# Performance work log

Hardware: AMD Instinct MI355X
Metric: run time of the kernel (lower is better)

Reference implementation:

```python
import jax, jax.numpy as jnp
import numpy as np

B, S, H, NH = 2, 2048, 1024, 16
HD = H // NH  # 64


def setup_inputs() -> dict:
    key = jax.random.key(0)
    ks = jax.random.split(key, 12)
    sc = 0.02
    return {
        "query": jax.random.normal(ks[0], (B, S, H), dtype=jnp.float32),
        "key": jax.random.normal(ks[1], (B, S, H), dtype=jnp.float32),
        "value": jax.random.normal(ks[2], (B, S, H), dtype=jnp.float32),
        "attention_mask": jnp.zeros((B, S, S), dtype=jnp.float32),
        "Wq": jax.random.normal(ks[3], (H, H), dtype=jnp.float32) * sc,
        "bq": jnp.zeros((H,), dtype=jnp.float32),
        "Wk": jax.random.normal(ks[4], (H, H), dtype=jnp.float32) * sc,
        "bk": jnp.zeros((H,), dtype=jnp.float32),
        "Wv": jax.random.normal(ks[5], (H, H), dtype=jnp.float32) * sc,
        "bv": jnp.zeros((H,), dtype=jnp.float32),
        "Wo": jax.random.normal(ks[6], (H, H), dtype=jnp.float32) * sc,
        "bo": jnp.zeros((H,), dtype=jnp.float32),
    }


def reference(query, key, value, attention_mask, Wq, bq, Wk, bk, Wv, bv, Wo, bo):
    b = query.shape[0]
    # linear projections
    q = query @ Wq + bq
    k = key @ Wk + bk
    v = value @ Wv + bv
    # [b, s, h] -> [b, nh, s, hd]
    def split_heads(x):
        return x.reshape(b, -1, NH, HD).transpose(0, 2, 1, 3)
    q, k, v = split_heads(q), split_heads(k), split_heads(v)
    # scaled dot-product attention with materialized score matrix (faithful)
    scores = jnp.einsum("bhqd,bhkd->bhqk", q, k) / jnp.sqrt(jnp.float32(HD))
    scores = scores + attention_mask[:, None, :, :]
    weights = jax.nn.softmax(scores, axis=-1)  # dropout p=0 (eval)
    out = jnp.einsum("bhqk,bhkd->bhqd", weights, v)
    out = out.transpose(0, 2, 1, 3).reshape(b, -1, H)
    return out @ Wo + bo
```

## Files before the change

### kernel.cpp

```cpp
#include <hip/hip_runtime.h>
#include <hip/hip_bf16.h>
#include <math.h>

#define S_  2048
#define H_  1024
#define NH_ 16
#define HD_ 64
#define MM  4096
#define NB_ 2
#define NT_ (S_ / 64)
#define LOG2E 1.44269504088896340736f
#define SMFIX 32.0f

typedef __attribute__((ext_vector_type(8))) short bf16x8;
typedef __attribute__((ext_vector_type(4))) float f32x4;
typedef __attribute__((ext_vector_type(16))) float f32x16;
typedef __attribute__((ext_vector_type(4))) unsigned short us4;
typedef __attribute__((ext_vector_type(8))) unsigned short us8;
typedef __attribute__((ext_vector_type(2))) unsigned uint2v;

__device__ __forceinline__ void gld_lds16(const void* g, void* l) {
    __builtin_amdgcn_global_load_lds(
        (const __attribute__((address_space(1))) unsigned int*)g,
        (__attribute__((address_space(3))) unsigned int*)l, 16, 0, 0);
}

__device__ __forceinline__ unsigned short f2bf(float f) {
    union { float f; unsigned int u; } v; v.f = f;
    unsigned int r = v.u + 0x7FFFu + ((v.u >> 16) & 1u);
    return (unsigned short)(r >> 16);
}

__device__ __forceinline__ unsigned pkbf(float lo, float hi) {
    __hip_bfloat162 h = __float22bfloat162_rn(make_float2(lo, hi));
    unsigned u; __builtin_memcpy(&u, &h, 4); return u;
}

__device__ __forceinline__ float exp2_fast(float x) {
    float r; asm("v_exp_f32 %0, %1" : "=v"(r) : "v"(x)); return r;
}

__global__ __launch_bounds__(256)
void cvt_bf16_3(const float* __restrict__ s0, const float* __restrict__ s1,
                const float* __restrict__ s2, unsigned short* __restrict__ d0,
                unsigned short* __restrict__ d1, unsigned short* __restrict__ d2,
                int n8)
{
    const int z = blockIdx.y;
    const float* s = z == 0 ? s0 : z == 1 ? s1 : s2;
    unsigned short* d = z == 0 ? d0 : z == 1 ? d1 : d2;
    int i = blockIdx.x * 256 + threadIdx.x;
    if (i >= n8) return;
    float4 a = ((const float4*)s)[i * 2];
    float4 b = ((const float4*)s)[i * 2 + 1];
    union { unsigned u[4]; us8 v; } o;
    o.u[0] = pkbf(a.x, a.y); o.u[1] = pkbf(a.z, a.w);
    o.u[2] = pkbf(b.x, b.y); o.u[3] = pkbf(b.z, b.w);
    ((us8*)d)[i] = o.v;
}

__global__ __launch_bounds__(256)
void wtr_kernel(const float* __restrict__ W0, const float* __restrict__ W1,
                const float* __restrict__ W2, const float* __restrict__ W3,
                unsigned short* __restrict__ T0, unsigned short* __restrict__ T1,
                unsigned short* __restrict__ T2, unsigned short* __restrict__ T3)
{
    __shared__ float t[32][33];
    const float* W = blockIdx.z == 0 ? W0 : blockIdx.z == 1 ? W1 : blockIdx.z == 2 ? W2 : W3;
    unsigned short* T = blockIdx.z == 0 ? T0 : blockIdx.z == 1 ? T1 : blockIdx.z == 2 ? T2 : T3;
    const int n0 = blockIdx.x * 32, k0 = blockIdx.y * 32;
    const int tx = threadIdx.x & 31, ty = threadIdx.x >> 5;
    #pragma unroll
    for (int u = 0; u < 4; u++)
        t[ty + u * 8][tx] = W[(size_t)(k0 + ty + u * 8) * H_ + n0 + tx];
    __syncthreads();
    #pragma unroll
    for (int u = 0; u < 4; u++)
        T[(size_t)(n0 + ty + u * 8) * H_ + k0 + tx] = f2bf(t[tx][ty + u * 8]);
}

__global__ __launch_bounds__(256)
void mtr_kernel(const float* __restrict__ M, unsigned short* __restrict__ MT2)
{
    __shared__ float t[64][33];
    const int q0 = blockIdx.x * 64, t2 = blockIdx.y, b = blockIdx.z;
    const int kv0 = (t2 >> 1) * 64 + (t2 & 1) * 32;
    const float* Mb = M + (size_t)b * S_ * S_;
    const int tid = threadIdx.x;

    #pragma unroll
    for (int u = 0; u < 2; u++) {
        const int f4 = tid + u * 256;
        const int r = f4 >> 3, c = (f4 & 7) * 4;
        float4 v = *(const float4*)(Mb + (size_t)(q0 + r) * S_ + kv0 + c);
        t[r][c + 0] = v.x; t[r][c + 1] = v.y; t[r][c + 2] = v.z; t[r][c + 3] = v.w;
    }
    __syncthreads();

    const int lg2 = tid >> 7, rem = tid & 127;
    const int q = rem >> 1, half = rem & 1;
    union { unsigned u[4]; us8 v; } o;
    #pragma unroll
    for (int w = 0; w < 4; w++) {
        const int i0 = half * 8 + 2 * w;
        const int kc0 = (i0 & 3) + 8 * (i0 >> 2) + 4 * lg2;
        const int i1 = i0 + 1;
        const int kc1 = (i1 & 3) + 8 * (i1 >> 2) + 4 * lg2;
        o.u[w] = pkbf(fmaf(t[q][kc0], LOG2E, -SMFIX),
                      fmaf(t[q][kc1], LOG2E, -SMFIX));
    }
    const size_t flat = ((((size_t)b * 64 + t2) * 2 + lg2) * 2048 + (q0 + q)) * 16 + half * 8;
    *(us8*)(MT2 + flat) = o.v;
}

__device__ __forceinline__
void gemm_body(const unsigned short* __restrict__ A, const unsigned short* __restrict__ Bt,
               const float* __restrict__ bias, void* __restrict__ out, float scale, int epi)
{
    __shared__ __align__(16) unsigned short As[128 * 64];
    __shared__ __align__(16) unsigned short Bs[128 * 64];

    const int tid = threadIdx.x;
    const int lane = tid & 63, w = tid >> 6;
    const int lane16 = lane & 15, lg = lane >> 4;
    const int wm = w & 1, wn = w >> 1;
    const int n0 = blockIdx.x * 128, m0 = blockIdx.y * 128;

    f32x4 acc[4][4];
    #pragma unroll
    for (int m = 0; m < 4; m++)
        #pragma unroll
        for (int n = 0; n < 4; n++) acc[m][n] = (f32x4){0.f, 0.f, 0.f, 0.f};

    auto stage = [&](int kt) {
        #pragma unroll
        for (int u = 0; u < 4; u++) {
            const int seg = w * 4 + u;
            const int L = seg * 1024 + lane * 16;
            const int row = L >> 7;
            const int blk = (L >> 4) & 7;
            const int goff = kt * 64 + ((blk ^ (row & 7)) << 3);
            gld_lds16(A  + (size_t)(m0 + row) * 1024 + goff, (char*)As + L);
            gld_lds16(Bt + (size_t)(n0 + row) * 1024 + goff, (char*)Bs + L);
        }
    };

    stage(0);
    for (int kt = 0; kt < 16; kt++) {
        __syncthreads();
        #pragma unroll
        for (int ks = 0; ks < 2; ks++) {
            const int kb = ks * 64 + lg * 16;
            bf16x8 a[4], b[4];
            #pragma unroll
            for (int m = 0; m < 4; m++) {
                const int row = wm * 64 + m * 16 + lane16;
                a[m] = *(const bf16x8*)((const char*)As + row * 128 + (kb ^ ((row & 7) << 4)));
            }
            #pragma unroll
            for (int n = 0; n < 4; n++) {
                const int row = wn * 64 + n * 16 + lane16;
                b[n] = *(const bf16x8*)((const char*)Bs + row * 128 + (kb ^ ((row & 7) << 4)));
            }
            #pragma unroll
            for (int m = 0; m < 4; m++)
                #pragma unroll
                for (int n = 0; n < 4; n++)
                    acc[m][n] = __builtin_amdgcn_mfma_f32_16x16x32_bf16(a[m], b[n], acc[m][n], 0, 0, 0);
        }
        __syncthreads();
        if (kt + 1 < 16) stage(kt + 1);
    }

    #pragma unroll
    for (int n = 0; n < 4; n++) {
        const int col = n0 + wn * 64 + n * 16 + lane16;
        const float bs = bias[col];
        #pragma unroll
        for (int m = 0; m < 4; m++) {
            const int rowb = m0 + wm * 64 + m * 16 + lg * 4;
            if (epi == 0) {
                const int nh = col >> 6, hd = col & 63;
                #pragma unroll
                for (int j = 0; j < 4; j++) {
                    const int row = rowb + j;
                    const int bb = row >> 11, s = row & 2047;
                    ((unsigned short*)out)[((((size_t)bb * NH_ + nh) * S_ + s) << 6) + hd] =
                        f2bf((acc[m][n][j] + bs) * scale);
                }
            } else if (epi == 1) {
                const int nh = col >> 6, hd = col & 63;
                const int bb = rowb >> 11, s = rowb & 2047;
                us4 o;
                #pragma unroll
                for (int j = 0; j < 4; j++) o[j] = f2bf(acc[m][n][j] + bs);
                *(us4*)&((unsigned short*)out)[((((size_t)bb * NH_ + nh) * HD_ + hd) << 11) + s] = o;
            } else {
                #pragma unroll
                for (int j = 0; j < 4; j++)
                    ((float*)out)[(size_t)(rowb + j) * H_ + col] = acc[m][n][j] + bs;
            }
        }
    }
}

__global__ __launch_bounds__(256)
void gemm_qkv(const unsigned short* __restrict__ Xq, const unsigned short* __restrict__ Xk,
              const unsigned short* __restrict__ Xv,
              const unsigned short* __restrict__ Wtq, const unsigned short* __restrict__ Wtk,
              const unsigned short* __restrict__ Wtv,
              const float* __restrict__ bq, const float* __restrict__ bk,
              const float* __restrict__ bv,
              unsigned short* __restrict__ qh, unsigned short* __restrict__ kh,
              unsigned short* __restrict__ vt, float qscale)
{
    const int z = blockIdx.z;
    const unsigned short* A  = z == 0 ? Xq : z == 1 ? Xk : Xv;
    const unsigned short* Bt = z == 0 ? Wtq : z == 1 ? Wtk : Wtv;
    const float* bias        = z == 0 ? bq : z == 1 ? bk : bv;
    void* out                = z == 0 ? (void*)qh : z == 1 ? (void*)kh : (void*)vt;
    gemm_body(A, Bt, bias, out, z == 0 ? qscale : 1.0f, z == 2 ? 1 : 0);
}

__global__ __launch_bounds__(256)
void gemm_out(const unsigned short* __restrict__ A, const unsigned short* __restrict__ Bt,
              const float* __restrict__ bias, float* __restrict__ out)
{
    gemm_body(A, Bt, bias, out, 1.0f, 2);
}

__global__ __launch_bounds__(256, 2)
void mfma_attn(const unsigned short* __restrict__ qh, const unsigned short* __restrict__ kh,
               const unsigned short* __restrict__ vt, const unsigned short* __restrict__ maskT,
               unsigned short* __restrict__ ao)
{
    __shared__ __align__(16) unsigned short Ks[2][64 * 64];
    __shared__ __align__(16) unsigned short Vs[2][64 * 64];

    const int tid = threadIdx.x;
    const int lane = tid & 63, wq = tid >> 6;
    const int l31 = lane & 31, lg2 = lane >> 5;
    const int qt = blockIdx.x, h = blockIdx.y, bz = blockIdx.z;
    const int q = qt * 128 + wq * 32 + l31;

    const unsigned short* Kb = kh + ((size_t)(bz * NH_ + h) * S_) * HD_;
    const unsigned short* Vb = vt + ((size_t)(bz * NH_ + h) * HD_) * S_;
    const unsigned short* MT2b = maskT + (size_t)bz * S_ * S_;

    bf16x8 qfrag[4];
    {
        const unsigned short* Qrow = qh + (((size_t)(bz * NH_ + h) * S_) + q) * HD_;
        #pragma unroll
        for (int s = 0; s < 4; s++)
            qfrag[s] = *(const bf16x8*)(Qrow + s * 16 + lg2 * 8);
    }

    auto stageKV = [&](int t) {
        const int buf = t & 1;
        #pragma unroll
        for (int u = 0; u < 2; u++) {
            const int L = u * 4096 + tid * 16;
            const int row = L >> 7, blk = (L >> 4) & 7;
            const int off = (blk ^ (row & 7)) << 3;
            gld_lds16(Kb + (size_t)(t * 64 + row) * HD_ + off, (char*)&Ks[buf][0] + L);
            gld_lds16(Vb + (size_t)row * S_ + t * 64 + off,    (char*)&Vs[buf][0] + L);
        }
    };
    stageKV(0);

    us8 mpA[2][2], mpB[2][2];
    auto loadMT = [&](int t, us8 (&mp)[2][2]) {
        #pragma unroll
        for (int bb = 0; bb < 2; bb++) {
            const unsigned short* src = MT2b +
                ((((size_t)(t * 2 + bb)) * 2 + lg2) * 2048 + q) * 16;
            mp[bb][0] = *(const us8*)(src);
            mp[bb][1] = *(const us8*)(src + 8);
        }
    };
    loadMT(0, mpA);

    __syncthreads();

    f32x16 oacc[2];
    #pragma unroll
    for (int db = 0; db < 2; db++)
        #pragma unroll
        for (int i = 0; i < 16; i++) oacc[db][i] = 0.f;
    float l_run = 0.f;

    auto tile = [&](int t, us8 (&Mc)[2][2], us8 (&Mn)[2][2]) {
        if (t) __syncthreads();
        const int buf = t & 1;

        if (t + 1 < NT_) { stageKV(t + 1); loadMT(t + 1, Mn); }

        f32x16 sc[2];
        __builtin_amdgcn_s_setprio(1);
        #pragma unroll
        for (int bb = 0; bb < 2; bb++) {
            f32x16 a;
            #pragma unroll
            for (int i = 0; i < 16; i++) a[i] = 0.f;
            #pragma unroll
            for (int s = 0; s < 4; s++) {
                const int row = bb * 32 + l31;
                bf16x8 kf = *(const bf16x8*)((const char*)&Ks[buf][0] + row * 128 +
                                             ((s * 32 + lg2 * 16) ^ ((row & 7) << 4)));
                a = __builtin_amdgcn_mfma_f32_32x32x16_bf16(kf, qfrag[s], a, 0, 0, 0);
            }
            sc[bb] = a;
        }
        __builtin_amdgcn_s_setprio(0);

        #pragma unroll
        for (int bb = 0; bb < 2; bb++) {
            union { us8 v; unsigned u[4]; } h0, h1;
            h0.v = Mc[bb][0]; h1.v = Mc[bb][1];
            #pragma unroll
            for (int i = 0; i < 16; i++) {
                const unsigned wrd = (i < 8) ? h0.u[i >> 1] : h1.u[(i - 8) >> 1];
                const float mf = __uint_as_float((i & 1) ? (wrd & 0xFFFF0000u)
                                                         : (wrd << 16));
                sc[bb][i] = exp2_fast(sc[bb][i] + mf);
            }
        }
        float s8[8];
        #pragma unroll
        for (int i = 0; i < 8; i++)
            s8[i] = (sc[0][i] + sc[0][i + 8]) + (sc[1][i] + sc[1][i + 8]);
        l_run += ((s8[0] + s8[1]) + (s8[2] + s8[3])) + ((s8[4] + s8[5]) + (s8[6] + s8[7]));

        bf16x8 pfrag[4];
        #pragma unroll
        for (int bb = 0; bb < 2; bb++)
            #pragma unroll
            for (int g = 0; g < 2; g++) {
                const int o = g * 8;
                unsigned X0 = pkbf(sc[bb][o + 0], sc[bb][o + 1]);
                unsigned X1 = pkbf(sc[bb][o + 2], sc[bb][o + 3]);
                unsigned Y0 = pkbf(sc[bb][o + 4], sc[bb][o + 5]);
                unsigned Y1 = pkbf(sc[bb][o + 6], sc[bb][o + 7]);
                uint2v r0 = __builtin_amdgcn_permlane32_swap(X0, Y0, false, false);
                uint2v r1 = __builtin_amdgcn_permlane32_swap(X1, Y1, false, false);
                union { unsigned u[4]; bf16x8 v; } P;
                P.u[0] = r0.x; P.u[1] = r1.x; P.u[2] = r0.y; P.u[3] = r1.y;
                pfrag[bb * 2 + g] = P.v;
            }

        __builtin_amdgcn_s_setprio(1);
        #pragma unroll
        for (int s = 0; s < 4; s++)
            #pragma unroll
            for (int db = 0; db < 2; db++) {
                const int row = db * 32 + l31;
                bf16x8 vf = *(const bf16x8*)((const char*)&Vs[buf][0] + row * 128 +
                                             ((s * 32 + lg2 * 16) ^ ((row & 7) << 4)));
                oacc[db] = __builtin_amdgcn_mfma_f32_32x32x16_bf16(vf, pfrag[s], oacc[db], 0, 0, 0);
            }
        __builtin_amdgcn_s_setprio(0);
    };

    for (int tt = 0; tt < NT_; tt += 2) {
        tile(tt,     mpA, mpB);
        tile(tt + 1, mpB, mpA);
    }

    l_run += __shfl_xor(l_run, 32, 64);
    const float inv = 1.0f / l_run;
    unsigned short* aoq = ao + ((size_t)(bz * S_ + q)) * H_ + h * HD_;
    #pragma unroll
    for (int db = 0; db < 2; db++)
        #pragma unroll
        for (int m = 0; m < 4; m++) {
            us4 o = { f2bf(oacc[db][m * 4 + 0] * inv), f2bf(oacc[db][m * 4 + 1] * inv),
                      f2bf(oacc[db][m * 4 + 2] * inv), f2bf(oacc[db][m * 4 + 3] * inv) };
            *(us4*)&aoq[db * 32 + m * 8 + lg2 * 4] = o;
        }
}

extern "C" void kernel_launch(void* const* d_in, const int* in_sizes, int n_in,
                              void* d_out, int out_size, void* d_ws, size_t ws_size,
                              hipStream_t stream)
{
    (void)in_sizes; (void)n_in; (void)out_size; (void)ws_size;

    const float* query = (const float*)d_in[0];
    const float* key   = (const float*)d_in[1];
    const float* value = (const float*)d_in[2];
    const float* mask  = (const float*)d_in[3];
    const float* Wq    = (const float*)d_in[4];
    const float* bq    = (const float*)d_in[5];
    const float* Wk    = (const float*)d_in[6];
    const float* bk    = (const float*)d_in[7];
    const float* Wv    = (const float*)d_in[8];
    const float* bv    = (const float*)d_in[9];
    const float* Wo    = (const float*)d_in[10];
    const float* bo    = (const float*)d_in[11];

    unsigned short* ws = (unsigned short*)d_ws;
    const size_t MH = (size_t)MM * H_;
    const size_t WW = (size_t)H_ * H_;
    unsigned short* Xq  = ws;
    unsigned short* Xk  = Xq + MH;
    unsigned short* Xv  = Xk + MH;
    unsigned short* Wtq = Xv + MH;
    unsigned short* Wtk = Wtq + WW;
    unsigned short* Wtv = Wtk + WW;
    unsigned short* Wto = Wtv + WW;
    unsigned short* qh  = Wto + WW;
    unsigned short* kh  = qh + MH;
    unsigned short* vt  = kh + MH;
    unsigned short* ao  = vt + MH;
    unsigned short* maskT = Xq;

    const int n8 = (int)(MH / 8);
    cvt_bf16_3<<<dim3(n8 / 256, 3), 256, 0, stream>>>(query, key, value, Xq, Xk, Xv, n8);
    wtr_kernel<<<dim3(32, 32, 4), 256, 0, stream>>>(Wq, Wk, Wv, Wo, Wtq, Wtk, Wtv, Wto);

    gemm_qkv<<<dim3(8, 32, 3), 256, 0, stream>>>(Xq, Xk, Xv, Wtq, Wtk, Wtv,
                                                 bq, bk, bv, qh, kh, vt, 0.125f * LOG2E);

    mtr_kernel<<<dim3(S_ / 64, 64, NB_), 256, 0, stream>>>(mask, maskT);

    mfma_attn<<<dim3(S_ / 128, NH_, NB_), 256, 0, stream>>>(qh, kh, vt, maskT, ao);

    gemm_out<<<dim3(8, 32), 256, 0, stream>>>(ao, Wto, bo, (float*)d_out);
}
```

Baseline: 148.7 us.

## Software-pipeline attention so next tile's QK^T overlaps current softmax and PV

Splits K and V staging into separate loads and restructures the attention loop so the QK^T MFMAs for tile t+1 are issued before the exp/pack/PV work of tile t. K is prefetched two tiles ahead and V one tile ahead, and score registers are double-buffered. The goal is to let matrix-core work overlap the exp and permlane VALU phase instead of running them back to back. The cost is an extra set of 32 score accumulators per lane, which raises register pressure and may reduce occupancy. The schedule also gains an extra prologue QK pass and its own barrier.

```diff
diff --git a/kernel.cpp b/kernel.cpp
--- a/kernel.cpp
+++ b/kernel.cpp
@@ -255,18 +255,24 @@
             qfrag[s] = *(const bf16x8*)(Qrow + s * 16 + lg2 * 8);
     }
 
-    auto stageKV = [&](int t) {
-        const int buf = t & 1;
+    auto stageK = [&](int t) {
         #pragma unroll
         for (int u = 0; u < 2; u++) {
             const int L = u * 4096 + tid * 16;
             const int row = L >> 7, blk = (L >> 4) & 7;
             const int off = (blk ^ (row & 7)) << 3;
-            gld_lds16(Kb + (size_t)(t * 64 + row) * HD_ + off, (char*)&Ks[buf][0] + L);
-            gld_lds16(Vb + (size_t)row * S_ + t * 64 + off,    (char*)&Vs[buf][0] + L);
-        }
-    };
-    stageKV(0);
+            gld_lds16(Kb + (size_t)(t * 64 + row) * HD_ + off, (char*)&Ks[t & 1][0] + L);
+        }
+    };
+    auto stageV = [&](int t) {
+        #pragma unroll
+        for (int u = 0; u < 2; u++) {
+            const int L = u * 4096 + tid * 16;
+            const int row = L >> 7, blk = (L >> 4) & 7;
+            const int off = (blk ^ (row & 7)) << 3;
+            gld_lds16(Vb + (size_t)row * S_ + t * 64 + off, (char*)&Vs[t & 1][0] + L);
+        }
+    };
 
     us8 mpA[2][2], mpB[2][2];
     auto loadMT = [&](int t, us8 (&mp)[2][2]) {
@@ -278,24 +284,9 @@
             mp[bb][1] = *(const us8*)(src + 8);
         }
     };
-    loadMT(0, mpA);
-
-    __syncthreads();
-
-    f32x16 oacc[2];
-    #pragma unroll
-    for (int db = 0; db < 2; db++)
-        #pragma unroll
-        for (int i = 0; i < 16; i++) oacc[db][i] = 0.f;
-    float l_run = 0.f;
-
-    auto tile = [&](int t, us8 (&Mc)[2][2], us8 (&Mn)[2][2]) {
-        if (t) __syncthreads();
+
+    auto qk = [&](int t, f32x16 (&sc)[2]) {
         const int buf = t & 1;
-
-        if (t + 1 < NT_) { stageKV(t + 1); loadMT(t + 1, Mn); }
-
-        f32x16 sc[2];
         __builtin_amdgcn_s_setprio(1);
         #pragma unroll
         for (int bb = 0; bb < 2; bb++) {
@@ -312,23 +303,47 @@
             sc[bb] = a;
         }
         __builtin_amdgcn_s_setprio(0);
+    };
+
+    f32x16 scA[2], scB[2];
+    f32x16 oacc[2];
+    #pragma unroll
+    for (int db = 0; db < 2; db++)
+        #pragma unroll
+        for (int i = 0; i < 16; i++) oacc[db][i] = 0.f;
+    float l_run = 0.f;
+
+    stageK(0); stageV(0); stageK(1);
+    loadMT(0, mpA);
+    __syncthreads();
+    qk(0, scA);
+    __syncthreads();
+
+    auto half = [&](int t, f32x16 (&scCur)[2], f32x16 (&scNext)[2],
+                    us8 (&mpCur)[2][2], us8 (&mpNext)[2][2]) {
+        if (t + 2 < NT_) stageK(t + 2);
+        if (t + 1 < NT_) {
+            stageV(t + 1);
+            loadMT(t + 1, mpNext);
+            qk(t + 1, scNext);
+        }
 
         #pragma unroll
         for (int bb = 0; bb < 2; bb++) {
             union { us8 v; unsigned u[4]; } h0, h1;
-            h0.v = Mc[bb][0]; h1.v = Mc[bb][1];
+            h0.v = mpCur[bb][0]; h1.v = mpCur[bb][1];
             #pragma unroll
             for (int i = 0; i < 16; i++) {
                 const unsigned wrd = (i < 8) ? h0.u[i >> 1] : h1.u[(i - 8) >> 1];
                 const float mf = __uint_as_float((i & 1) ? (wrd & 0xFFFF0000u)
                                                          : (wrd << 16));
-                sc[bb][i] = exp2_fast(sc[bb][i] + mf);
+                scCur[bb][i] = exp2_fast(scCur[bb][i] + mf);
             }
         }
         float s8[8];
         #pragma unroll
         for (int i = 0; i < 8; i++)
-            s8[i] = (sc[0][i] + sc[0][i + 8]) + (sc[1][i] + sc[1][i + 8]);
+            s8[i] = (scCur[0][i] + scCur[0][i + 8]) + (scCur[1][i] + scCur[1][i + 8]);
         l_run += ((s8[0] + s8[1]) + (s8[2] + s8[3])) + ((s8[4] + s8[5]) + (s8[6] + s8[7]));
 
         bf16x8 pfrag[4];
@@ -337,10 +352,10 @@
             #pragma unroll
             for (int g = 0; g < 2; g++) {
                 const int o = g * 8;
-                unsigned X0 = pkbf(sc[bb][o + 0], sc[bb][o + 1]);
-                unsigned X1 = pkbf(sc[bb][o + 2], sc[bb][o + 3]);
-                unsigned Y0 = pkbf(sc[bb][o + 4], sc[bb][o + 5]);
-                unsigned Y1 = pkbf(sc[bb][o + 6], sc[bb][o + 7]);
+                unsigned X0 = pkbf(scCur[bb][o + 0], scCur[bb][o + 1]);
+                unsigned X1 = pkbf(scCur[bb][o + 2], scCur[bb][o + 3]);
+                unsigned Y0 = pkbf(scCur[bb][o + 4], scCur[bb][o + 5]);
+                unsigned Y1 = pkbf(scCur[bb][o + 6], scCur[bb][o + 7]);
                 uint2v r0 = __builtin_amdgcn_permlane32_swap(X0, Y0, false, false);
                 uint2v r1 = __builtin_amdgcn_permlane32_swap(X1, Y1, false, false);
                 union { unsigned u[4]; bf16x8 v; } P;
@@ -354,16 +369,18 @@
             #pragma unroll
             for (int db = 0; db < 2; db++) {
                 const int row = db * 32 + l31;
-                bf16x8 vf = *(const bf16x8*)((const char*)&Vs[buf][0] + row * 128 +
+                bf16x8 vf = *(const bf16x8*)((const char*)&Vs[t & 1][0] + row * 128 +
                                              ((s * 32 + lg2 * 16) ^ ((row & 7) << 4)));
                 oacc[db] = __builtin_amdgcn_mfma_f32_32x32x16_bf16(vf, pfrag[s], oacc[db], 0, 0, 0);
             }
         __builtin_amdgcn_s_setprio(0);
+
+        __syncthreads();
     };
 
     for (int tt = 0; tt < NT_; tt += 2) {
-        tile(tt,     mpA, mpB);
-        tile(tt + 1, mpB, mpA);
+        half(tt,     scA, scB, mpA, mpB);
+        half(tt + 1, scB, scA, mpB, mpA);
     }
 
     l_run += __shfl_xor(l_run, 32, 64);
```

Result: no change. 149.0 us (+0.2%).
